# Performance work log

Measured on AMD Instinct MI355X. Metric: run time of the kernel, lower is better.

## Reference

```python
import jax, jax.numpy as jnp
import numpy as np

DIM = 1024
HEADS = 16
HEAD_DIM = DIM // HEADS


def setup_inputs() -> dict:
    key = jax.random.key(0)
    ks = jax.random.split(key, 5)
    x = jax.random.normal(ks[0], (4, 2048, DIM), dtype=jnp.float32)
    # torch Linear params: weight [out, in], bias [out]
    qkv_w = jax.random.normal(ks[1], (3 * DIM, DIM), dtype=jnp.float32) * (1.0 / np.sqrt(DIM))
    qkv_b = jax.random.normal(ks[2], (3 * DIM,), dtype=jnp.float32) * 0.01
    out_w = jax.random.normal(ks[3], (DIM, DIM), dtype=jnp.float32) * (1.0 / np.sqrt(DIM))
    out_b = jax.random.normal(ks[4], (DIM,), dtype=jnp.float32) * 0.01
    return {"x": x, "qkv_w": qkv_w, "qkv_b": qkv_b, "out_w": out_w, "out_b": out_b}


def reference(x, qkv_w, qkv_b, out_w, out_b):
    b, s, d = x.shape
    scale = 1.0 / np.sqrt(HEAD_DIM)
    qkv = x @ qkv_w.T + qkv_b                      # [b, s, 3d]
    qkv = qkv.reshape(b, s, 3, HEADS, HEAD_DIM)
    qkv = jnp.transpose(qkv, (2, 0, 3, 1, 4))      # [3, b, h, s, hd]
    q, k, v = qkv[0], qkv[1], qkv[2]
    attn = jnp.einsum('bhqd,bhkd->bhqk', q, k) * scale
    attn = jax.nn.softmax(attn, axis=-1)
    out = jnp.einsum('bhqk,bhkd->bhqd', attn, v)   # [b, h, s, hd]
    out = jnp.transpose(out, (0, 2, 1, 3)).reshape(b, s, d)
    return out @ out_w.T + out_b
```

## Files before the change

kernel.cpp:

```cpp
#include <hip/hip_runtime.h>

namespace {

constexpr int DIMC  = 1024;
constexpr int HEADS = 16;
constexpr int HD    = 64;
constexpr int BATCH = 4;
constexpr int SEQ   = 2048;
constexpr float SC2 = 0.18033688011112042f;

typedef __attribute__((ext_vector_type(8))) short short8;
typedef __attribute__((ext_vector_type(4))) float f32x4;

__device__ __forceinline__ unsigned short f2bf(float f) {
    union { float f; unsigned u; } v; v.f = f;
    unsigned r = v.u + 0x7fffu + ((v.u >> 16) & 1u);
    return (unsigned short)(r >> 16);
}

__device__ __forceinline__ float fexp2(float x) {
    float r;
    asm("v_exp_f32 %0, %1" : "=v"(r) : "v"(x));
    return r;
}

__device__ __forceinline__ void gl16(const unsigned short* gsrc, const unsigned short* ldst) {
    __builtin_amdgcn_global_load_lds(
        (const __attribute__((address_space(1))) void*)gsrc,
        (__attribute__((address_space(3))) void*)ldst, 16, 0, 0);
}

__global__ __launch_bounds__(256) void cvt3_f32_bf16(
    const float* __restrict__ x,  const float* __restrict__ wq,
    const float* __restrict__ wo,
    unsigned short* __restrict__ xb, unsigned short* __restrict__ wqb,
    unsigned short* __restrict__ wob)
{
    constexpr int N0 = 8192*1024/8;
    constexpr int N1 = 3072*1024/8;
    constexpr int N2 = 1024*1024/8;
    for (int i = blockIdx.x * blockDim.x + threadIdx.x; i < N0 + N1 + N2;
         i += gridDim.x * blockDim.x) {
        const float* src; unsigned short* dst; int j;
        if (i < N0)           { src = x;  dst = xb;  j = i; }
        else if (i < N0 + N1) { src = wq; dst = wqb; j = i - N0; }
        else                  { src = wo; dst = wob; j = i - N0 - N1; }
        const float4 a = ((const float4*)src)[2*j];
        const float4 b = ((const float4*)src)[2*j + 1];
        union { unsigned short s[8]; uint4 u; } p;
        p.s[0]=f2bf(a.x); p.s[1]=f2bf(a.y); p.s[2]=f2bf(a.z); p.s[3]=f2bf(a.w);
        p.s[4]=f2bf(b.x); p.s[5]=f2bf(b.y); p.s[6]=f2bf(b.z); p.s[7]=f2bf(b.w);
        ((uint4*)dst)[j] = p.u;
    }
}

template<int OUT_BF16>
__global__ __launch_bounds__(256) void gemm_bf16_mfma(
    const unsigned short* __restrict__ A, const unsigned short* __restrict__ W,
    const float* __restrict__ bias, void* __restrict__ Cout,
    int M, int N, int K)
{
    __shared__ __align__(16) char lds[32768];
    unsigned short* base = (unsigned short*)lds;

    const int tid = threadIdx.x;
    const int w = tid >> 6, l = tid & 63;
    const int wr = w >> 1, wc = w & 1;
    const int fr = l & 15, fq = l >> 4;
    const int row0 = blockIdx.y * 128, col0 = blockIdx.x * 128;

    const int sr0 = (w*2 + 0)*16 + (l >> 2);
    const int sr1 = (w*2 + 1)*16 + (l >> 2);
    const int skz = (((l & 3) ^ ((l >> 3) & 3))) * 8;

    const unsigned short* Ab0 = A + (size_t)(row0 + sr0)*K + skz;
    const unsigned short* Ab1 = A + (size_t)(row0 + sr1)*K + skz;
    const unsigned short* Wb0 = W + (size_t)(col0 + sr0)*K + skz;
    const unsigned short* Wb1 = W + (size_t)(col0 + sr1)*K + skz;

    f32x4 acc[4][4];
#pragma unroll
    for (int mi = 0; mi < 4; ++mi)
#pragma unroll
        for (int ni = 0; ni < 4; ++ni)
#pragma unroll
            for (int r = 0; r < 4; ++r) acc[mi][ni][r] = 0.f;

    const int cfa = (fq ^ ((fr >> 1) & 3)) * 8;

    auto stage = [&](int k0, int buf) {
        unsigned short* Ad = base + buf*8192;
        unsigned short* Wd = Ad + 4096;
        gl16(Ab0 + k0, Ad + (w*2 + 0)*512);
        gl16(Ab1 + k0, Ad + (w*2 + 1)*512);
        gl16(Wb0 + k0, Wd + (w*2 + 0)*512);
        gl16(Wb1 + k0, Wd + (w*2 + 1)*512);
    };

    stage(0, 0);
    for (int k0 = 0; k0 < K; k0 += 32) {
        const int buf = (k0 >> 5) & 1;
        __syncthreads();
        if (k0 + 32 < K) stage(k0 + 32, buf ^ 1);

        const unsigned short* Ac = base + buf*8192;
        const unsigned short* Wc = Ac + 4096;
        short8 af[4], bf[4];
#pragma unroll
        for (int mi = 0; mi < 4; ++mi)
            af[mi] = *(const short8*)(Ac + (wr*64 + mi*16 + fr)*32 + cfa);
#pragma unroll
        for (int ni = 0; ni < 4; ++ni)
            bf[ni] = *(const short8*)(Wc + (wc*64 + ni*16 + fr)*32 + cfa);
#pragma unroll
        for (int mi = 0; mi < 4; ++mi)
#pragma unroll
            for (int ni = 0; ni < 4; ++ni)
                acc[mi][ni] = __builtin_amdgcn_mfma_f32_16x16x32_bf16(
                    af[mi], bf[ni], acc[mi][ni], 0, 0, 0);
    }

    float bv[4];
#pragma unroll
    for (int ni = 0; ni < 4; ++ni) bv[ni] = bias[col0 + wc*64 + ni*16 + fr];
#pragma unroll
    for (int mi = 0; mi < 4; ++mi)
#pragma unroll
        for (int ni = 0; ni < 4; ++ni)
#pragma unroll
            for (int r = 0; r < 4; ++r) acc[mi][ni][r] += bv[ni];

    __syncthreads();
    float* rp = (float*)lds + w*1088;
    const int orow = l >> 2, oc = (l & 3) * 16;
#pragma unroll
    for (int mi = 0; mi < 4; ++mi) {
#pragma unroll
        for (int ni = 0; ni < 4; ++ni)
#pragma unroll
            for (int r = 0; r < 4; ++r)
                rp[(fq*4 + r)*68 + ni*16 + fr] = acc[mi][ni][r];
        float vrow[16];
#pragma unroll
        for (int j = 0; j < 4; ++j)
            *(f32x4*)&vrow[j*4] = *(const f32x4*)&rp[orow*68 + oc + j*4];
        const size_t grow = (size_t)(row0 + wr*64 + mi*16 + orow);
        const int    gcol = col0 + wc*64 + oc;
        if (OUT_BF16) {
            union { unsigned short s[16]; uint4 u[2]; } pk;
#pragma unroll
            for (int j = 0; j < 16; ++j) pk.s[j] = f2bf(vrow[j]);
            uint4* dst = (uint4*)((unsigned short*)Cout + grow*N + gcol);
            dst[0] = pk.u[0]; dst[1] = pk.u[1];
        } else {
            float* dst = (float*)Cout + grow*N + gcol;
#pragma unroll
            for (int j = 0; j < 4; ++j)
                *(f32x4*)(dst + j*4) = *(const f32x4*)&vrow[j*4];
        }
    }
}

__global__ __launch_bounds__(256) void transpose_v(
    const unsigned short* __restrict__ qkvb, unsigned short* __restrict__ vt)
{
    __shared__ __align__(16) unsigned short T[64*72];
    const int tid = threadIdx.x;
    const int s0 = blockIdx.x * 64, h = blockIdx.y, b = blockIdx.z;
    const unsigned short* src = qkvb + (size_t)b*SEQ*3072 + 2048 + h*64;

    const int r = tid >> 2, c0 = (tid & 3) * 16;
    uint4 u0 = *(const uint4*)(src + (size_t)(s0 + r)*3072 + c0);
    uint4 u1 = *(const uint4*)(src + (size_t)(s0 + r)*3072 + c0 + 8);
    unsigned short e[16];
    *(uint4*)&e[0] = u0; *(uint4*)&e[8] = u1;
#pragma unroll
    for (int i = 0; i < 16; ++i) T[(c0 + i)*72 + r] = e[i];
    __syncthreads();
    const int d = tid >> 2, ss = (tid & 3) * 16;
    uint4 w0 = *(const uint4*)(&T[d*72 + ss]);
    uint4 w1 = *(const uint4*)(&T[d*72 + ss + 8]);
    unsigned short* dst = vt + ((size_t)((b*16 + h)*64 + d))*SEQ + s0 + ss;
    *(uint4*)dst = w0; *(uint4*)(dst + 8) = w1;
}

__global__ __launch_bounds__(256) void attn_mfma(
    const unsigned short* __restrict__ qkvb,
    const unsigned short* __restrict__ vt,
    unsigned short* __restrict__ ctxb)
{
    __shared__ __align__(16) char pool[51200];
    unsigned short* Kb0 = (unsigned short*)pool;
    unsigned short* Vb0 = Kb0 + 8192;
    unsigned short* Pl  = Kb0 + 16384;

    const int tid = threadIdx.x, w = tid >> 6, l = tid & 63;
    const int fr = l & 15, fq = l >> 4;

    const int bid = blockIdx.x;
    const int nid = (bid & 7) * 128 + (bid >> 3);
    const int b  = nid >> 8;
    const int h  = (nid >> 4) & 15;
    const int q0 = (nid & 15) * 128;
    const int wq = q0 + w*32;

    const unsigned short* qb = qkvb + (size_t)b*SEQ*3072 + h*64;
    const unsigned short* kb = qb + 1024;
    const unsigned short* vb = vt + (size_t)((b*16 + h)*64)*SEQ;

    auto scale8 = [](short8 v) -> short8 {
        union { short8 s; unsigned u[4]; } in, out;
        in.s = v;
#pragma unroll
        for (int i = 0; i < 4; ++i) {
            const float lo = __uint_as_float(in.u[i] << 16) * SC2;
            const float hi = __uint_as_float(in.u[i] & 0xffff0000u) * SC2;
            unsigned r;
            asm("v_cvt_pk_bf16_f32 %0, %1, %2" : "=v"(r) : "v"(lo), "v"(hi));
            out.u[i] = r;
        }
        return out.s;
    };
    short8 qf[2][2];
#pragma unroll
    for (int mf = 0; mf < 2; ++mf)
#pragma unroll
        for (int kk = 0; kk < 2; ++kk)
            qf[mf][kk] = scale8(*(const short8*)(qb + (size_t)(wq + mf*16 + fr)*3072
                                                 + kk*32 + fq*8));

    short8 ones;
#pragma unroll
    for (int i = 0; i < 8; ++i) ones[i] = (short)0x3F80;

    f32x4 z4;
#pragma unroll
    for (int r = 0; r < 4; ++r) z4[r] = 0.f;

    f32x4 o[2][4];
    f32x4 ol[2];
#pragma unroll
    for (int mf = 0; mf < 2; ++mf) {
#pragma unroll
        for (int df = 0; df < 4; ++df)
#pragma unroll
            for (int r = 0; r < 4; ++r) o[mf][df][r] = 0.f;
#pragma unroll
        for (int r = 0; r < 4; ++r) ol[mf][r] = 0.f;
    }

    const int srA = (w*2 + 0)*8 + (l >> 3);
    const int srB = (w*2 + 1)*8 + (l >> 3);
    const int scz = ((l & 7) ^ (l >> 3)) * 8;
    unsigned short* Pw = Pl + w*2304;

    const int c0e = (fq ^ (fr & 7)) * 8;
    const int c1e = c0e ^ 32;

    auto stage = [&](int kv0, int buf) {
        unsigned short* Kd = Kb0 + buf*4096;
        unsigned short* Vd = Vb0 + buf*4096;
        gl16(kb + (size_t)(kv0 + srA)*3072 + scz, Kd + (w*2 + 0)*512);
        gl16(kb + (size_t)(kv0 + srB)*3072 + scz, Kd + (w*2 + 1)*512);
        gl16(vb + (size_t)srA*SEQ + kv0 + scz,    Vd + (w*2 + 0)*512);
        gl16(vb + (size_t)srB*SEQ + kv0 + scz,    Vd + (w*2 + 1)*512);
    };

    stage(0, 0);
    for (int kv0 = 0; kv0 < SEQ; kv0 += 64) {
        const int buf = (kv0 >> 6) & 1;
        __syncthreads();
        if (kv0 + 64 < SEQ) stage(kv0 + 64, buf ^ 1);

        const unsigned short* Kc = Kb0 + buf*4096;
        const unsigned short* Vc = Vb0 + buf*4096;

        short8 vf[4][2];
#pragma unroll
        for (int df = 0; df < 4; ++df) {
            vf[df][0] = *(const short8*)(Vc + (df*16 + fr)*64 + c0e);
            vf[df][1] = *(const short8*)(Vc + (df*16 + fr)*64 + c1e);
        }

        f32x4 s[2][4];
#pragma unroll
        for (int nf = 0; nf < 4; ++nf) {
            const short8 k0f = *(const short8*)(Kc + (nf*16 + fr)*64 + c0e);
            const short8 k1f = *(const short8*)(Kc + (nf*16 + fr)*64 + c1e);
#pragma unroll
            for (int mf = 0; mf < 2; ++mf) {
                s[mf][nf] = __builtin_amdgcn_mfma_f32_16x16x32_bf16(k0f, qf[mf][0], z4, 0,0,0);
                s[mf][nf] = __builtin_amdgcn_mfma_f32_16x16x32_bf16(k1f, qf[mf][1], s[mf][nf], 0,0,0);
            }
        }

#pragma unroll
        for (int mf = 0; mf < 2; ++mf)
#pragma unroll
            for (int nf = 0; nf < 4; ++nf) {
                const float p0 = fexp2(s[mf][nf][0]);
                const float p1 = fexp2(s[mf][nf][1]);
                const float p2 = fexp2(s[mf][nf][2]);
                const float p3 = fexp2(s[mf][nf][3]);
                unsigned u0, u1;
                asm("v_cvt_pk_bf16_f32 %0, %1, %2" : "=v"(u0) : "v"(p0), "v"(p1));
                asm("v_cvt_pk_bf16_f32 %0, %1, %2" : "=v"(u1) : "v"(p2), "v"(p3));
                uint2 pw; pw.x = u0; pw.y = u1;
                *(uint2*)(Pw + (mf*16 + fr)*72 + nf*16 + fq*4) = pw;
            }

        short8 pa[2][2];
#pragma unroll
        for (int mf = 0; mf < 2; ++mf)
#pragma unroll
            for (int kk = 0; kk < 2; ++kk)
                pa[mf][kk] = *(const short8*)(Pw + (mf*16 + fr)*72 + kk*32 + fq*8);
#pragma unroll
        for (int mf = 0; mf < 2; ++mf) {
            ol[mf] = __builtin_amdgcn_mfma_f32_16x16x32_bf16(ones, pa[mf][0], ol[mf], 0,0,0);
            ol[mf] = __builtin_amdgcn_mfma_f32_16x16x32_bf16(ones, pa[mf][1], ol[mf], 0,0,0);
        }
#pragma unroll
        for (int df = 0; df < 4; ++df)
#pragma unroll
            for (int mf = 0; mf < 2; ++mf) {
                o[mf][df] = __builtin_amdgcn_mfma_f32_16x16x32_bf16(vf[df][0], pa[mf][0], o[mf][df], 0,0,0);
                o[mf][df] = __builtin_amdgcn_mfma_f32_16x16x32_bf16(vf[df][1], pa[mf][1], o[mf][df], 0,0,0);
            }
    }

    __syncthreads();
    float* rp = (float*)(pool + w*8704);
    const float inv0 = 1.f / ol[0][0], inv1 = 1.f / ol[1][0];
#pragma unroll
    for (int df = 0; df < 4; ++df) {
        f32x4 v0 = o[0][df] * inv0;
        f32x4 v1 = o[1][df] * inv1;
        *(f32x4*)&rp[(fr)*68      + df*16 + fq*4] = v0;
        *(f32x4*)&rp[(16 + fr)*68 + df*16 + fq*4] = v1;
    }
    const int orow = l >> 1, oc = (l & 1)*32;
    float vr[32];
#pragma unroll
    for (int j = 0; j < 8; ++j)
        *(f32x4*)&vr[j*4] = *(const f32x4*)&rp[orow*68 + oc + j*4];
    union { unsigned short s[32]; uint4 u[4]; } pk;
#pragma unroll
    for (int j = 0; j < 32; ++j) pk.s[j] = f2bf(vr[j]);
    unsigned short* dst = ctxb + (size_t)(b*SEQ + q0 + w*32 + orow)*DIMC + h*64 + oc;
#pragma unroll
    for (int j = 0; j < 4; ++j) *((uint4*)dst + j) = pk.u[j];
}

}

extern "C" void kernel_launch(void* const* d_in, const int* in_sizes, int n_in,
                              void* d_out, int out_size, void* d_ws, size_t ws_size,
                              hipStream_t stream)
{
    const float* x     = (const float*)d_in[0];
    const float* qkv_w = (const float*)d_in[1];
    const float* qkv_b = (const float*)d_in[2];
    const float* out_w = (const float*)d_in[3];
    const float* out_b = (const float*)d_in[4];

    unsigned short* xb   = (unsigned short*)d_ws;
    unsigned short* wqb  = xb   + (size_t)8192*1024;
    unsigned short* wob  = wqb  + (size_t)3072*1024;
    unsigned short* qkvb = wob  + (size_t)1024*1024;
    unsigned short* vtw  = qkvb + (size_t)8192*3072;
    unsigned short* ctxb = vtw  + (size_t)4096*2048;

    cvt3_f32_bf16<<<2048, 256, 0, stream>>>(x, qkv_w, out_w, xb, wqb, wob);

    gemm_bf16_mfma<1><<<dim3(24, 64), 256, 0, stream>>>(
        xb, wqb, qkv_b, (void*)qkvb, 8192, 3072, 1024);

    transpose_v<<<dim3(SEQ/64, HEADS, BATCH), 256, 0, stream>>>(qkvb, vtw);

    attn_mfma<<<dim3(1024), 256, 0, stream>>>(qkvb, vtw, ctxb);

    gemm_bf16_mfma<0><<<dim3(8, 64), 256, 0, stream>>>(
        ctxb, wob, out_b, d_out, 8192, 1024, 1024);
}
```

Baseline: 200.7 us.

## Fuse V transpose into QKV GEMM epilogue and swizzle GEMM block order

The QKV projection GEMM now writes the V columns straight into the transposed [b,h,d,s] layout from its LDS staging buffer, so the separate transpose_v kernel and its extra read and write of V are gone. Both GEMMs switch to a 1D grid whose block index is remapped across 8 groups, which spreads neighbouring tiles over XCDs and changes L2 locality. The V-path stores are 32-byte rows per lane at a stride of SEQ, which may coalesce less well than the previous row-major stores.

```diff
diff --git a/kernel.cpp b/kernel.cpp
--- a/kernel.cpp
+++ b/kernel.cpp
@@ -54,11 +54,12 @@
     }
 }
 
-template<int OUT_BF16>
+template<int OUT_MODE>
 __global__ __launch_bounds__(256) void gemm_bf16_mfma(
     const unsigned short* __restrict__ A, const unsigned short* __restrict__ W,
     const float* __restrict__ bias, void* __restrict__ Cout,
-    int M, int N, int K)
+    unsigned short* __restrict__ vt,
+    int M, int N, int K, int nbx)
 {
     __shared__ __align__(16) char lds[32768];
     unsigned short* base = (unsigned short*)lds;
@@ -67,7 +68,11 @@
     const int w = tid >> 6, l = tid & 63;
     const int wr = w >> 1, wc = w & 1;
     const int fr = l & 15, fq = l >> 4;
-    const int row0 = blockIdx.y * 128, col0 = blockIdx.x * 128;
+
+    const int qx  = gridDim.x >> 3;
+    const int nid = (blockIdx.x & 7) * qx + (blockIdx.x >> 3);
+    const int bx  = nid % nbx, by = nid / nbx;
+    const int row0 = by * 128, col0 = bx * 128;
 
     const int sr0 = (w*2 + 0)*16 + (l >> 2);
     const int sr1 = (w*2 + 1)*16 + (l >> 2);
@@ -133,6 +138,9 @@
     __syncthreads();
     float* rp = (float*)lds + w*1088;
     const int orow = l >> 2, oc = (l & 3) * 16;
+    const bool vmode = (OUT_MODE == 2) && (col0 >= 2048);
+    const int hh = vmode ? ((col0 + wc*64 - 2048) >> 6) : 0;
+
 #pragma unroll
     for (int mi = 0; mi < 4; ++mi) {
 #pragma unroll
@@ -140,48 +148,39 @@
 #pragma unroll
             for (int r = 0; r < 4; ++r)
                 rp[(fq*4 + r)*68 + ni*16 + fr] = acc[mi][ni][r];
-        float vrow[16];
-#pragma unroll
-        for (int j = 0; j < 4; ++j)
-            *(f32x4*)&vrow[j*4] = *(const f32x4*)&rp[orow*68 + oc + j*4];
-        const size_t grow = (size_t)(row0 + wr*64 + mi*16 + orow);
-        const int    gcol = col0 + wc*64 + oc;
-        if (OUT_BF16) {
+        if (vmode) {
+            float cv[16];
+#pragma unroll
+            for (int j = 0; j < 16; ++j) cv[j] = rp[j*68 + l];
             union { unsigned short s[16]; uint4 u[2]; } pk;
 #pragma unroll
-            for (int j = 0; j < 16; ++j) pk.s[j] = f2bf(vrow[j]);
-            uint4* dst = (uint4*)((unsigned short*)Cout + grow*N + gcol);
-            dst[0] = pk.u[0]; dst[1] = pk.u[1];
+            for (int j = 0; j < 16; ++j) pk.s[j] = f2bf(cv[j]);
+            const int srow0 = row0 + wr*64 + mi*16;
+            const int bb = srow0 >> 11, ss = srow0 & 2047;
+            unsigned short* dst = vt + ((size_t)((bb*16 + hh)*64 + l))*SEQ + ss;
+            ((uint4*)dst)[0] = pk.u[0];
+            ((uint4*)dst)[1] = pk.u[1];
         } else {
-            float* dst = (float*)Cout + grow*N + gcol;
+            float vrow[16];
 #pragma unroll
             for (int j = 0; j < 4; ++j)
-                *(f32x4*)(dst + j*4) = *(const f32x4*)&vrow[j*4];
-        }
-    }
-}
-
-__global__ __launch_bounds__(256) void transpose_v(
-    const unsigned short* __restrict__ qkvb, unsigned short* __restrict__ vt)
-{
-    __shared__ __align__(16) unsigned short T[64*72];
-    const int tid = threadIdx.x;
-    const int s0 = blockIdx.x * 64, h = blockIdx.y, b = blockIdx.z;
-    const unsigned short* src = qkvb + (size_t)b*SEQ*3072 + 2048 + h*64;
-
-    const int r = tid >> 2, c0 = (tid & 3) * 16;
-    uint4 u0 = *(const uint4*)(src + (size_t)(s0 + r)*3072 + c0);
-    uint4 u1 = *(const uint4*)(src + (size_t)(s0 + r)*3072 + c0 + 8);
-    unsigned short e[16];
-    *(uint4*)&e[0] = u0; *(uint4*)&e[8] = u1;
-#pragma unroll
-    for (int i = 0; i < 16; ++i) T[(c0 + i)*72 + r] = e[i];
-    __syncthreads();
-    const int d = tid >> 2, ss = (tid & 3) * 16;
-    uint4 w0 = *(const uint4*)(&T[d*72 + ss]);
-    uint4 w1 = *(const uint4*)(&T[d*72 + ss + 8]);
-    unsigned short* dst = vt + ((size_t)((b*16 + h)*64 + d))*SEQ + s0 + ss;
-    *(uint4*)dst = w0; *(uint4*)(dst + 8) = w1;
+                *(f32x4*)&vrow[j*4] = *(const f32x4*)&rp[orow*68 + oc + j*4];
+            const size_t grow = (size_t)(row0 + wr*64 + mi*16 + orow);
+            const int    gcol = col0 + wc*64 + oc;
+            if (OUT_MODE == 2) {
+                union { unsigned short s[16]; uint4 u[2]; } pk;
+#pragma unroll
+                for (int j = 0; j < 16; ++j) pk.s[j] = f2bf(vrow[j]);
+                uint4* dst = (uint4*)((unsigned short*)Cout + grow*N + gcol);
+                dst[0] = pk.u[0]; dst[1] = pk.u[1];
+            } else {
+                float* dst = (float*)Cout + grow*N + gcol;
+#pragma unroll
+                for (int j = 0; j < 4; ++j)
+                    *(f32x4*)(dst + j*4) = *(const f32x4*)&vrow[j*4];
+            }
+        }
+    }
 }
 
 __global__ __launch_bounds__(256) void attn_mfma(
@@ -373,13 +372,11 @@
 
     cvt3_f32_bf16<<<2048, 256, 0, stream>>>(x, qkv_w, out_w, xb, wqb, wob);
 
-    gemm_bf16_mfma<1><<<dim3(24, 64), 256, 0, stream>>>(
-        xb, wqb, qkv_b, (void*)qkvb, 8192, 3072, 1024);
-
-    transpose_v<<<dim3(SEQ/64, HEADS, BATCH), 256, 0, stream>>>(qkvb, vtw);
+    gemm_bf16_mfma<2><<<dim3(1536), 256, 0, stream>>>(
+        xb, wqb, qkv_b, (void*)qkvb, vtw, 8192, 3072, 1024, 24);
 
     attn_mfma<<<dim3(1024), 256, 0, stream>>>(qkvb, vtw, ctxb);
 
-    gemm_bf16_mfma<0><<<dim3(8, 64), 256, 0, stream>>>(
-        ctxb, wob, out_b, d_out, 8192, 1024, 1024);
-}
+    gemm_bf16_mfma<0><<<dim3(512), 256, 0, stream>>>(
+        ctxb, wob, out_b, d_out, nullptr, 8192, 1024, 1024, 8);
+}
```

Result: no change. 201.7 us (+0.5%).
